# Optimization experiments

Measured on AMD Instinct MI355X. Metric: run time of the kernel, lower is better.

## Reference

```python
import jax, jax.numpy as jnp
import numpy as np

B, S, H, L = 64, 512, 768, 9


def setup_inputs() -> dict:
    key = jax.random.key(0)
    ks = jax.random.split(key, 8)
    hidden = jax.random.normal(ks[0], (B, S, H), jnp.float32)
    lengths = jax.random.randint(ks[1], (B,), S // 2, S + 1)
    attention_mask = (jnp.arange(S)[None, :] < lengths[:, None]).astype(jnp.int32)
    labels = jax.random.randint(ks[2], (B, S), 0, L)
    # sprinkle some -100 ignore labels like HF datasets do
    ignore = jax.random.uniform(ks[3], (B, S)) < 0.05
    labels = jnp.where(ignore, -100, labels)
    W = jax.random.normal(ks[4], (H, L), jnp.float32) * 0.02
    b = jnp.zeros((L,), jnp.float32)
    start_transitions = jax.random.uniform(ks[5], (L,), jnp.float32, -0.1, 0.1)
    end_transitions = jax.random.uniform(ks[6], (L,), jnp.float32, -0.1, 0.1)
    transitions = jax.random.uniform(ks[7], (L, L), jnp.float32, -0.1, 0.1)
    return dict(hidden=hidden, attention_mask=attention_mask, labels=labels, W=W, b=b,
                start_transitions=start_transitions, end_transitions=end_transitions,
                transitions=transitions)


def _crf_numerator(emissions, tags, maskf, start_t, end_t, trans):
    # score of the gold tag sequence (torchcrf _compute_score)
    first = start_t[tags[:, 0]] + jnp.take_along_axis(emissions[:, 0], tags[:, 0:1], axis=1)[:, 0]
    em = jnp.take_along_axis(emissions, tags[..., None], axis=2)[..., 0]      # [B,S]
    tr = trans[tags[:, :-1], tags[:, 1:]]                                     # [B,S-1]
    score = first + jnp.sum((em[:, 1:] + tr) * maskf[:, 1:], axis=1)
    last_idx = (jnp.sum(maskf, axis=1).astype(jnp.int32) - 1)
    last_tags = jnp.take_along_axis(tags, last_idx[:, None], axis=1)[:, 0]
    return score + end_t[last_tags]


def _crf_lognorm(emissions, maskf, start_t, end_t, trans):
    # forward algorithm (torchcrf _compute_normalizer) as a lax.scan
    score0 = start_t[None, :] + emissions[:, 0]                               # [B,L]
    em_seq = jnp.transpose(emissions[:, 1:], (1, 0, 2))                       # [S-1,B,L]
    m_seq = maskf[:, 1:].T                                                    # [S-1,B]

    def step(score, xs):
        em_t, m_t = xs
        nxt = jax.nn.logsumexp(score[:, :, None] + trans[None] + em_t[:, None, :], axis=1)
        return jnp.where(m_t[:, None] > 0, nxt, score), None

    score, _ = jax.lax.scan(step, score0, (em_seq, m_seq))
    return jax.nn.logsumexp(score + end_t[None, :], axis=1)


def _viterbi(emissions, maskf, start_t, end_t, trans):
    score0 = start_t[None, :] + emissions[:, 0]                               # [B,L]
    em_seq = jnp.transpose(emissions[:, 1:], (1, 0, 2))
    m_seq = maskf[:, 1:].T

    def step(score, xs):
        em_t, m_t = xs
        cand = score[:, :, None] + trans[None]                                # [B,L,L]
        bp = jnp.argmax(cand, axis=1)                                         # [B,L]
        nxt = jnp.max(cand, axis=1) + em_t
        return jnp.where(m_t[:, None] > 0, nxt, score), bp

    score, history = jax.lax.scan(step, score0, (em_seq, m_seq))              # history [S-1,B,L]
    best_last = jnp.argmax(score + end_t[None, :], axis=1)                    # [B]

    def back(cur, xs):
        bp_t, m_t = xs
        prev = jnp.where(m_t > 0, jnp.take_along_axis(bp_t, cur[:, None], axis=1)[:, 0], cur)
        return prev, prev

    _, tags_rev = jax.lax.scan(back, best_last, (history[::-1], m_seq[::-1]))
    tags = jnp.concatenate([tags_rev[::-1].T, best_last[:, None]], axis=1)    # [B,S]
    return tags


def reference(hidden, attention_mask, labels, W, b, start_transitions, end_transitions, transitions):
    maskf = attention_mask.astype(hidden.dtype)                               # [B,S]
    logits = jnp.einsum('bsh,hl->bsl', hidden, W) + b                         # [B,S,L]
    safe_labels = jnp.where(labels == -100, 0, labels)
    num = _crf_numerator(logits, safe_labels, maskf, start_transitions, end_transitions, transitions)
    den = _crf_lognorm(logits, maskf, start_transitions, end_transitions, transitions)
    loss = -jnp.mean(num - den)                                               # -crf(..., reduction='mean')
    tags = _viterbi(logits, maskf, start_transitions, end_transitions, transitions)
    fake_logits = jax.nn.one_hot(tags, L, dtype=logits.dtype) * maskf[..., None]
    return loss, fake_logits
```

## Files before the change

### kernel.cpp

```cpp
#include <hip/hip_runtime.h>
#include <hip/hip_bf16.h>
#include <stdint.h>

constexpr int BB  = 64;
constexpr int SS  = 512;
constexpr int HH  = 768;
constexpr int NL  = 9;
constexpr int NROWS = BB * SS;
constexpr int EMN   = SS * NL;
constexpr int NSEG  = 8;
constexpr float NEG  = -1e30f;

__device__ __forceinline__ float readlane_f(float v, int lane) {
  union { float f; int i; } u;
  u.f = v;
  u.i = __builtin_amdgcn_readlane(u.i, lane);
  return u.f;
}

__global__ __launch_bounds__(256, 2) void logits_kernel(
    const float* __restrict__ hidden, const float* __restrict__ W,
    const float* __restrict__ bias, const int* __restrict__ mask,
    float* __restrict__ logits, int* __restrict__ lens) {
  const int lane = threadIdx.x & 63;
  const int wid  = blockIdx.x * 4 + (threadIdx.x >> 6);

  if (blockIdx.x < 64 && threadIdx.x < 64) {
    const int4* mp = (const int4*)(mask + blockIdx.x * SS);
    const int4 a = mp[threadIdx.x];
    const int4 c = mp[threadIdx.x + 64];
    int lsum = a.x + a.y + a.z + a.w + c.x + c.y + c.z + c.w;
#pragma unroll
    for (int off = 32; off >= 1; off >>= 1) lsum += __shfl_xor(lsum, off, 64);
    if (threadIdx.x == 0) lens[blockIdx.x] = lsum;
  }

  float w[3][4][NL];
#pragma unroll
  for (int j = 0; j < 3; ++j)
#pragma unroll
    for (int k = 0; k < 4; ++k) {
      const int r = lane * 4 + j * 256 + k;
#pragma unroll
      for (int l = 0; l < NL; ++l) w[j][k][l] = W[r * NL + l];
    }
  const float my_bias = (lane < NL) ? bias[lane] : 0.0f;

  float4 h[4][3];
#pragma unroll
  for (int r = 0; r < 4; ++r) {
    const float4* hp = (const float4*)(hidden + (size_t)(wid + r * 8192) * HH);
#pragma unroll
    for (int j = 0; j < 3; ++j) h[r][j] = hp[lane + j * 64];
  }
  float acc[4][NL];
#pragma unroll
  for (int r = 0; r < 4; ++r)
#pragma unroll
    for (int l = 0; l < NL; ++l) acc[r][l] = 0.0f;
#pragma unroll
  for (int r = 0; r < 4; ++r)
#pragma unroll
    for (int j = 0; j < 3; ++j)
#pragma unroll
      for (int l = 0; l < NL; ++l)
        acc[r][l] += h[r][j].x * w[j][0][l] + h[r][j].y * w[j][1][l] +
                     h[r][j].z * w[j][2][l] + h[r][j].w * w[j][3][l];
#pragma unroll
  for (int off = 32; off >= 1; off >>= 1)
#pragma unroll
    for (int r = 0; r < 4; ++r)
#pragma unroll
      for (int l = 0; l < NL; ++l)
        acc[r][l] += __shfl_xor(acc[r][l], off, 64);
  if (lane < NL) {
#pragma unroll
    for (int r = 0; r < 4; ++r) {
      float v = acc[r][0];
#pragma unroll
      for (int l = 1; l < NL; ++l) if (lane == l) v = acc[r][l];
      logits[(size_t)(wid + r * 8192) * NL + lane] = v + my_bias;
    }
  }
}

__global__ __launch_bounds__(64) void scan_kernel(
    const float* __restrict__ logits, const int* __restrict__ labels,
    const float* __restrict__ start_t, const float* __restrict__ end_t,
    const float* __restrict__ trans, float* __restrict__ out,
    float* __restrict__ num_den, const int* __restrict__ lens,
    float* __restrict__ segmat) {
  __shared__ unsigned char bp_s[EMN + 80];
  __shared__ unsigned char tags_s[SS];
  __shared__ int lab[SS];

  const int blk = blockIdx.x;
  const int tid = threadIdx.x;
  const int j   = (tid < NL) ? tid : NL - 1;

  if (blk < 64) {
    const int b   = blk;
    const int len = lens[b];
    const float* emb = logits + (size_t)b * EMN;
    float tc[NL];
#pragma unroll
    for (int i = 0; i < NL; ++i) tc[i] = trans[i * NL + j];
    float s[NL];
#pragma unroll
    for (int i = 0; i < NL; ++i) s[i] = start_t[i] + emb[i];
    float eA = emb[1 * NL + j], eB = emb[2 * NL + j];
    float eC = emb[3 * NL + j], eD = emb[4 * NL + j];
    for (int t = 1; t < len; ++t) {
      float c[NL];
#pragma unroll
      for (int i = 0; i < NL; ++i) c[i] = s[i] + tc[i];
      const float x01 = fmaxf(c[0], c[1]), x23 = fmaxf(c[2], c[3]);
      const float x45 = fmaxf(c[4], c[5]), x67 = fmaxf(c[6], c[7]);
      const float best = fmaxf(fmaxf(fmaxf(x01, x23), fmaxf(x45, x67)), c[8]);
      const float nxt = best + eA;
      {
        const bool b01 = c[0] >= c[1], b23 = c[2] >= c[3];
        const bool b45 = c[4] >= c[5], b67 = c[6] >= c[7];
        const float v01 = b01 ? c[0] : c[1]; const int i01 = b01 ? 0 : 1;
        const float v23 = b23 ? c[2] : c[3]; const int i23 = b23 ? 2 : 3;
        const float v45 = b45 ? c[4] : c[5]; const int i45 = b45 ? 4 : 5;
        const float v67 = b67 ? c[6] : c[7]; const int i67 = b67 ? 6 : 7;
        const bool bA = v01 >= v23, bB = v45 >= v67;
        const float vA = bA ? v01 : v23; const int iA = bA ? i01 : i23;
        const float vB = bB ? v45 : v67; const int iB = bB ? i45 : i67;
        const bool bC = vA >= vB;
        const float vC = bC ? vA : vB; const int iC = bC ? iA : iB;
        const bool bD = vC >= c[8];
        const int arg = bD ? iC : 8;
        bp_s[t * NL + tid] = (unsigned char)arg;
      }
#pragma unroll
      for (int i = 0; i < NL; ++i) s[i] = readlane_f(nxt, i);
      eA = eB; eB = eC; eC = eD;
      eD = emb[(t + 4) * NL + j];
    }
    float bv = s[0] + end_t[0];
    int   bl = 0;
#pragma unroll
    for (int i = 1; i < NL; ++i) {
      const float cc = s[i] + end_t[i];
      if (cc > bv) { bv = cc; bl = i; }
    }
    __syncthreads();

    uint64_t C = 0x876543210ULL;
#pragma unroll
    for (int k = 1; k <= 8; ++k) {
      const int t = 8 * tid + k;
      uint64_t nc = 0;
#pragma unroll
      for (int x = 0; x < 9; ++x) {
        const int g = bp_s[t * NL + x] & 15;
        nc |= ((C >> (4 * g)) & 15ULL) << (4 * x);
      }
      C = (t < len) ? nc : C;
    }
    const uint32_t Clo = (uint32_t)C, Chi = (uint32_t)(C >> 32);
    uint32_t cur = (uint32_t)bl;
    int bnd = 0;
#pragma unroll
    for (int c = 63; c >= 0; --c) {
      bnd = (tid == c) ? (int)cur : bnd;
      const uint32_t lo = (uint32_t)__builtin_amdgcn_readlane((int)Clo, c);
      const uint32_t hi = (uint32_t)__builtin_amdgcn_readlane((int)Chi, c);
      const uint64_t cc = ((uint64_t)hi << 32) | lo;
      cur = (uint32_t)((cc >> (4 * cur)) & 15u);
    }
    int tag = bnd;
#pragma unroll
    for (int k = 8; k >= 1; --k) {
      const int t = 8 * tid + k;
      const int tt = (t < 512) ? t : 511;
      const int nt = bp_s[tt * NL + tag];
      tag = (t < len) ? nt : tag;
      tags_s[t - 1] = (unsigned char)tag;
    }
    __syncthreads();
    for (int i = tid; i < EMN; i += 64) {
      const int t = i / NL;
      const int l = i - t * NL;
      out[1 + (size_t)b * EMN + i] =
          (t < len && l == (int)tags_s[t]) ? 1.0f : 0.0f;
    }

  } else if (blk < 128) {
    const int b   = blk - 64;
    const int len = lens[b];
    const float* emb = logits + (size_t)b * EMN;
    for (int t = tid; t < SS; t += 64) {
      const int v = labels[b * SS + t];
      lab[t] = (v == -100) ? 0 : v;
    }
    __syncthreads();
    float contrib = 0.0f;
    for (int t = tid; t < SS; t += 64) {
      if (t >= 1 && t < len)
        contrib += emb[t * NL + lab[t]] + trans[lab[t - 1] * NL + lab[t]];
    }
#pragma unroll
    for (int off = 32; off >= 1; off >>= 1)
      contrib += __shfl_xor(contrib, off, 64);
    if (tid == 0) {
      const int l0 = lab[0];
      num_den[b] = start_t[l0] + emb[l0] + contrib + end_t[lab[len - 1]];
    }

  } else {
    const int id   = blk - 128;
    const int pair = id / 3;
    const int wv   = id - pair * 3;
    const int b    = pair >> 3;
    const int sg   = pair & 7;
    const int e0   = 3 * wv;
    const int len  = lens[b];
    const float* emb = logits + (size_t)b * EMN;
    float tc[NL];
#pragma unroll
    for (int i = 0; i < NL; ++i) tc[i] = trans[i * NL + j];
    float s0[NL], s1[NL], s2[NL];
#pragma unroll
    for (int i = 0; i < NL; ++i) {
      s0[i] = (i == e0)     ? 0.0f : NEG;
      s1[i] = (i == e0 + 1) ? 0.0f : NEG;
      s2[i] = (i == e0 + 2) ? 0.0f : NEG;
    }
    float my0 = (j == e0)     ? 0.0f : NEG;
    float my1 = (j == e0 + 1) ? 0.0f : NEG;
    float my2 = (j == e0 + 2) ? 0.0f : NEG;
    const int tbeg  = 64 * sg + 1;
    const int tlast = (64 * sg + 64 < 511) ? 64 * sg + 64 : 511;
    float eA = emb[tbeg * NL + j],       eB = emb[(tbeg + 1) * NL + j];
    float eC = emb[(tbeg + 2) * NL + j], eD = emb[(tbeg + 3) * NL + j];
    for (int t = tbeg; t <= tlast; ++t) {
      if (t >= len) break;
      float c0[NL], c1[NL], c2[NL];
#pragma unroll
      for (int i = 0; i < NL; ++i) {
        c0[i] = s0[i] + tc[i];
        c1[i] = s1[i] + tc[i];
        c2[i] = s2[i] + tc[i];
      }
      const float m0 = fmaxf(fmaxf(fmaxf(fmaxf(c0[0], c0[1]), fmaxf(c0[2], c0[3])),
                                   fmaxf(fmaxf(c0[4], c0[5]), fmaxf(c0[6], c0[7]))), c0[8]);
      const float m1 = fmaxf(fmaxf(fmaxf(fmaxf(c1[0], c1[1]), fmaxf(c1[2], c1[3])),
                                   fmaxf(fmaxf(c1[4], c1[5]), fmaxf(c1[6], c1[7]))), c1[8]);
      const float m2 = fmaxf(fmaxf(fmaxf(fmaxf(c2[0], c2[1]), fmaxf(c2[2], c2[3])),
                                   fmaxf(fmaxf(c2[4], c2[5]), fmaxf(c2[6], c2[7]))), c2[8]);
      float u0 = 0.0f, u1 = 0.0f, u2 = 0.0f;
#pragma unroll
      for (int i = 0; i < NL; ++i) {
        u0 += __expf(c0[i] - m0);
        u1 += __expf(c1[i] - m1);
        u2 += __expf(c2[i] - m2);
      }
      my0 = m0 + __logf(u0) + eA;
      my1 = m1 + __logf(u1) + eA;
      my2 = m2 + __logf(u2) + eA;
#pragma unroll
      for (int i = 0; i < NL; ++i) {
        s0[i] = readlane_f(my0, i);
        s1[i] = readlane_f(my1, i);
        s2[i] = readlane_f(my2, i);
      }
      eA = eB; eB = eC; eC = eD;
      eD = emb[(t + 4) * NL + j];
    }
    if (tid < NL) {
      float* M = segmat + (size_t)(b * NSEG + sg) * 81;
      M[(e0    ) * NL + tid] = my0;
      M[(e0 + 1) * NL + tid] = my1;
      M[(e0 + 2) * NL + tid] = my2;
    }
  }
}

__global__ __launch_bounds__(64) void combine_kernel(
    const float* __restrict__ logits, const float* __restrict__ segmat,
    const float* __restrict__ start_t, const float* __restrict__ end_t,
    const float* __restrict__ num_den, float* __restrict__ out) {
  const int b   = blockIdx.x;
  const int tid = threadIdx.x;
  const int j   = (tid < NL) ? tid : NL - 1;
  float s[NL];
#pragma unroll
  for (int i = 0; i < NL; ++i) s[i] = start_t[i] + logits[(size_t)b * EMN + i];
  float mcur[NL], mnxt[NL];
  {
    const float* M = segmat + (size_t)(b * NSEG) * 81;
#pragma unroll
    for (int i = 0; i < NL; ++i) mcur[i] = M[i * NL + j];
  }
  for (int sg = 0; sg < NSEG; ++sg) {
    if (sg + 1 < NSEG) {
      const float* M = segmat + (size_t)(b * NSEG + sg + 1) * 81;
#pragma unroll
      for (int i = 0; i < NL; ++i) mnxt[i] = M[i * NL + j];
    }
    float c[NL];
#pragma unroll
    for (int i = 0; i < NL; ++i) c[i] = s[i] + mcur[i];
    const float x01 = fmaxf(c[0], c[1]), x23 = fmaxf(c[2], c[3]);
    const float x45 = fmaxf(c[4], c[5]), x67 = fmaxf(c[6], c[7]);
    const float m = fmaxf(fmaxf(fmaxf(x01, x23), fmaxf(x45, x67)), c[8]);
    float sum = 0.0f;
#pragma unroll
    for (int i = 0; i < NL; ++i) sum += __expf(c[i] - m);
    const float nxt = m + __logf(sum);
#pragma unroll
    for (int i = 0; i < NL; ++i) s[i] = readlane_f(nxt, i);
#pragma unroll
    for (int i = 0; i < NL; ++i) mcur[i] = mnxt[i];
  }
  float c[NL];
#pragma unroll
  for (int i = 0; i < NL; ++i) c[i] = s[i] + end_t[i];
  const float x01 = fmaxf(c[0], c[1]), x23 = fmaxf(c[2], c[3]);
  const float x45 = fmaxf(c[4], c[5]), x67 = fmaxf(c[6], c[7]);
  const float m = fmaxf(fmaxf(fmaxf(x01, x23), fmaxf(x45, x67)), c[8]);
  float sum = 0.0f;
#pragma unroll
  for (int i = 0; i < NL; ++i) sum += __expf(c[i] - m);
  if (tid == 0) {
    const float den = m + __logf(sum);
    atomicAdd(out, (den - num_den[b]) * (1.0f / 64.0f));
  }
}

extern "C" void kernel_launch(void* const* d_in, const int* in_sizes, int n_in,
                              void* d_out, int out_size, void* d_ws, size_t ws_size,
                              hipStream_t stream) {
  const float* hidden  = (const float*)d_in[0];
  const int*   mask    = (const int*)d_in[1];
  const int*   labels  = (const int*)d_in[2];
  const float* W       = (const float*)d_in[3];
  const float* bias    = (const float*)d_in[4];
  const float* start_t = (const float*)d_in[5];
  const float* end_t   = (const float*)d_in[6];
  const float* trans   = (const float*)d_in[7];
  float* out = (float*)d_out;

  float* logits  = (float*)d_ws;
  float* segmat  = logits + (size_t)NROWS * NL;
  float* num_den = segmat + (size_t)BB * NSEG * 81;
  int*   lens    = (int*)(num_den + 128);

  hipMemsetAsync(out, 0, sizeof(float), stream);
  logits_kernel<<<2048, 256, 0, stream>>>(hidden, W, bias, mask, logits, lens);
  scan_kernel<<<1664, 64, 0, stream>>>(logits, labels, start_t, end_t, trans,
                                       out, num_den, lens, segmat);
  combine_kernel<<<64, 64, 0, stream>>>(logits, segmat, start_t, end_t,
                                        num_den, out);
}
```

Measured before the change: 256.8 us.

## Stage Viterbi emissions in LDS, merge max/argmax, fold memset into kernel

The serial Viterbi blocks now copy their 512x9 emission slice into shared memory up front and read from LDS inside the sequential loop, so global-memory latency is taken off the per-step critical path. The separate max reduction and argmax tree are merged into one select tree, and these blocks raise their wave priority with s_setprio. The host memset that zeroes the output scalar is replaced by a store inside the logits kernel, and labels are stored as bytes in LDS. In exchange each block uses more shared memory and pays for an upfront copy plus a barrier.

```diff
diff --git a/kernel.cpp b/kernel.cpp
--- a/kernel.cpp
+++ b/kernel.cpp
@@ -21,9 +21,12 @@
 __global__ __launch_bounds__(256, 2) void logits_kernel(
     const float* __restrict__ hidden, const float* __restrict__ W,
     const float* __restrict__ bias, const int* __restrict__ mask,
-    float* __restrict__ logits, int* __restrict__ lens) {
+    float* __restrict__ logits, int* __restrict__ lens,
+    float* __restrict__ out) {
   const int lane = threadIdx.x & 63;
   const int wid  = blockIdx.x * 4 + (threadIdx.x >> 6);
+
+  if (blockIdx.x == 0 && threadIdx.x == 0) out[0] = 0.0f;
 
   if (blockIdx.x < 64 && threadIdx.x < 64) {
     const int4* mp = (const int4*)(mask + blockIdx.x * SS);
@@ -90,54 +93,61 @@
     const float* __restrict__ trans, float* __restrict__ out,
     float* __restrict__ num_den, const int* __restrict__ lens,
     float* __restrict__ segmat) {
+  __shared__ float4 embv[1161];
   __shared__ unsigned char bp_s[EMN + 80];
   __shared__ unsigned char tags_s[SS];
-  __shared__ int lab[SS];
+  __shared__ unsigned char lab[SS];
 
   const int blk = blockIdx.x;
   const int tid = threadIdx.x;
   const int j   = (tid < NL) ? tid : NL - 1;
 
   if (blk < 64) {
+    __builtin_amdgcn_s_setprio(1);
     const int b   = blk;
     const int len = lens[b];
     const float* emb = logits + (size_t)b * EMN;
+
+    {
+      const float4* src = (const float4*)emb;
+#pragma unroll
+      for (int i = 0; i < 18; ++i) embv[tid + i * 64] = src[tid + i * 64];
+    }
+    __syncthreads();
+    const float* emb_s = (const float*)embv;
+
     float tc[NL];
 #pragma unroll
     for (int i = 0; i < NL; ++i) tc[i] = trans[i * NL + j];
     float s[NL];
 #pragma unroll
-    for (int i = 0; i < NL; ++i) s[i] = start_t[i] + emb[i];
-    float eA = emb[1 * NL + j], eB = emb[2 * NL + j];
-    float eC = emb[3 * NL + j], eD = emb[4 * NL + j];
+    for (int i = 0; i < NL; ++i) s[i] = start_t[i] + emb_s[i];
+    float eA = emb_s[1 * NL + j], eB = emb_s[2 * NL + j];
+    float eC = emb_s[3 * NL + j], eD = emb_s[4 * NL + j];
     for (int t = 1; t < len; ++t) {
       float c[NL];
 #pragma unroll
       for (int i = 0; i < NL; ++i) c[i] = s[i] + tc[i];
-      const float x01 = fmaxf(c[0], c[1]), x23 = fmaxf(c[2], c[3]);
-      const float x45 = fmaxf(c[4], c[5]), x67 = fmaxf(c[6], c[7]);
-      const float best = fmaxf(fmaxf(fmaxf(x01, x23), fmaxf(x45, x67)), c[8]);
+      const bool b01 = c[0] >= c[1], b23 = c[2] >= c[3];
+      const bool b45 = c[4] >= c[5], b67 = c[6] >= c[7];
+      const float v01 = b01 ? c[0] : c[1]; const int i01 = b01 ? 0 : 1;
+      const float v23 = b23 ? c[2] : c[3]; const int i23 = b23 ? 2 : 3;
+      const float v45 = b45 ? c[4] : c[5]; const int i45 = b45 ? 4 : 5;
+      const float v67 = b67 ? c[6] : c[7]; const int i67 = b67 ? 6 : 7;
+      const bool bA = v01 >= v23, bB = v45 >= v67;
+      const float vA = bA ? v01 : v23; const int iA = bA ? i01 : i23;
+      const float vB = bB ? v45 : v67; const int iB = bB ? i45 : i67;
+      const bool bC = vA >= vB;
+      const float vC = bC ? vA : vB; const int iC = bC ? iA : iB;
+      const bool bD = vC >= c[8];
+      const float best = bD ? vC : c[8];
+      const int   arg  = bD ? iC : 8;
+      bp_s[t * NL + tid] = (unsigned char)arg;
       const float nxt = best + eA;
-      {
-        const bool b01 = c[0] >= c[1], b23 = c[2] >= c[3];
-        const bool b45 = c[4] >= c[5], b67 = c[6] >= c[7];
-        const float v01 = b01 ? c[0] : c[1]; const int i01 = b01 ? 0 : 1;
-        const float v23 = b23 ? c[2] : c[3]; const int i23 = b23 ? 2 : 3;
-        const float v45 = b45 ? c[4] : c[5]; const int i45 = b45 ? 4 : 5;
-        const float v67 = b67 ? c[6] : c[7]; const int i67 = b67 ? 6 : 7;
-        const bool bA = v01 >= v23, bB = v45 >= v67;
-        const float vA = bA ? v01 : v23; const int iA = bA ? i01 : i23;
-        const float vB = bB ? v45 : v67; const int iB = bB ? i45 : i67;
-        const bool bC = vA >= vB;
-        const float vC = bC ? vA : vB; const int iC = bC ? iA : iB;
-        const bool bD = vC >= c[8];
-        const int arg = bD ? iC : 8;
-        bp_s[t * NL + tid] = (unsigned char)arg;
-      }
 #pragma unroll
       for (int i = 0; i < NL; ++i) s[i] = readlane_f(nxt, i);
       eA = eB; eB = eC; eC = eD;
-      eD = emb[(t + 4) * NL + j];
+      eD = emb_s[(t + 4) * NL + j];
     }
     float bv = s[0] + end_t[0];
     int   bl = 0;
@@ -194,7 +204,7 @@
     const float* emb = logits + (size_t)b * EMN;
     for (int t = tid; t < SS; t += 64) {
       const int v = labels[b * SS + t];
-      lab[t] = (v == -100) ? 0 : v;
+      lab[t] = (unsigned char)((v == -100) ? 0 : v);
     }
     __syncthreads();
     float contrib = 0.0f;
@@ -349,8 +359,7 @@
   float* num_den = segmat + (size_t)BB * NSEG * 81;
   int*   lens    = (int*)(num_den + 128);
 
-  hipMemsetAsync(out, 0, sizeof(float), stream);
-  logits_kernel<<<2048, 256, 0, stream>>>(hidden, W, bias, mask, logits, lens);
+  logits_kernel<<<2048, 256, 0, stream>>>(hidden, W, bias, mask, logits, lens, out);
   scan_kernel<<<1664, 64, 0, stream>>>(logits, labels, start_t, end_t, trans,
                                        out, num_den, lens, segmat);
   combine_kernel<<<64, 64, 0, stream>>>(logits, segmat, start_t, end_t,
```

New measurement: 256.6 us. About the same (-0.1%).
